# Performance work log

Measured on AMD Instinct MI355X. Metric: run time of the kernel, lower is better.

Reference implementation:

```python
import jax, jax.numpy as jnp
import numpy as np

WS = 7          # window size
DISP = 3        # WS // 2 cyclic shift displacement
HEADS = 3
HD = 32         # head dim
DIM = 96        # hidden dim (= HEADS*HD)
DS = 4          # patch-merging downscale factor
NWH = 16        # windows per spatial dim after merging (112/7)
SCALE = HD ** -0.5


def _rel_indices(ws):
    idx = np.array([[x, y] for x in range(ws) for y in range(ws)])
    return idx[None, :, :] - idx[:, None, :] + ws - 1  # (ws^2, ws^2, 2)


def _shift_mask(ws, disp, nwh, nww):
    n = ws * ws
    ul = np.zeros((n, n), np.float32)
    ul[-disp * ws:, :-disp * ws] = -np.inf
    ul[:-disp * ws, -disp * ws:] = -np.inf
    lr = np.zeros((ws, ws, ws, ws), np.float32)
    lr[:, -disp:, :, :-disp] = -np.inf
    lr[:, :-disp, :, -disp:] = -np.inf
    lr = lr.reshape(n, n)
    m = np.zeros((nwh * nww, n, n), np.float32)
    m[-nww:] += ul            # last row of windows: upper/lower mask
    m[nww - 1::nww] += lr     # last column of windows: left/right mask
    return m

REL = jnp.asarray(_rel_indices(WS))                       # (49,49,2) int
SHIFT_MASK = jnp.asarray(_shift_mask(WS, DISP, NWH, NWH))  # (256,49,49)


def _layernorm(x, g, b):
    mu = jnp.mean(x, axis=-1, keepdims=True)
    var = jnp.var(x, axis=-1, keepdims=True)
    return (x - mu) * jax.lax.rsqrt(var + 1e-5) * g + b


def _window_attention(y, wqkv, pos_tab, wo, bo, shifted):
    # y: (b, nh, nw, DIM)
    if shifted:
        y = jnp.roll(y, (-DISP, -DISP), axis=(1, 2))
    b, nh, nw, _ = y.shape
    nwh, nww = nh // WS, nw // WS
    qkv = y @ wqkv  # (b, nh, nw, 3*DIM); last dim layout [q|k|v]
    qkv = qkv.reshape(b, nwh, WS, nww, WS, 3, HEADS, HD)
    qkv = qkv.transpose(5, 0, 6, 1, 3, 2, 4, 7).reshape(3, b, HEADS, nwh * nww, WS * WS, HD)
    q, k, v = qkv[0], qkv[1], qkv[2]
    dots = jnp.einsum('bhwid,bhwjd->bhwij', q, k) * SCALE  # (b,h,nwin,49,49)
    dots = dots + pos_tab[REL[..., 0], REL[..., 1]]        # relative pos bias
    if shifted:
        dots = dots + SHIFT_MASK[None, None]
    attn = jax.nn.softmax(dots, axis=-1)
    o = jnp.einsum('bhwij,bhwjd->bhwid', attn, v)
    o = o.reshape(b, HEADS, nwh, nww, WS, WS, HD)
    o = o.transpose(0, 2, 4, 3, 5, 1, 6).reshape(b, nh, nw, HEADS * HD)
    o = o @ wo + bo
    if shifted:
        o = jnp.roll(o, (DISP, DISP), axis=(1, 2))
    return o


def setup_inputs() -> dict:
    key = jax.random.key(0)
    ks = jax.random.split(key, 8)
    B, C, H, W = 16, 3, 448, 448
    s = 0.02
    return {
        'x': jax.random.normal(ks[0], (B, C, H, W), jnp.float32),
        'pm_w': jax.random.normal(ks[1], (C * DS * DS, DIM), jnp.float32) * s,
        'pm_b': jnp.zeros((DIM,), jnp.float32),
        'ln1_g': jnp.ones((2, DIM), jnp.float32),
        'ln1_b': jnp.zeros((2, DIM), jnp.float32),
        'qkv_w': jax.random.normal(ks[2], (2, DIM, 3 * HEADS * HD), jnp.float32) * s,
        'pos': jax.random.normal(ks[3], (2, 2 * WS - 1, 2 * WS - 1), jnp.float32),
        'out_w': jax.random.normal(ks[4], (2, HEADS * HD, DIM), jnp.float32) * s,
        'out_b': jnp.zeros((2, DIM), jnp.float32),
        'ln2_g': jnp.ones((2, DIM), jnp.float32),
        'ln2_b': jnp.zeros((2, DIM), jnp.float32),
        'ff1_w': jax.random.normal(ks[5], (2, DIM, 4 * DIM), jnp.float32) * s,
        'ff1_b': jnp.zeros((2, 4 * DIM), jnp.float32),
        'ff2_w': jax.random.normal(ks[6], (2, 4 * DIM, DIM), jnp.float32) * s,
        'ff2_b': jnp.zeros((2, DIM), jnp.float32),
    }


def reference(x, pm_w, pm_b, ln1_g, ln1_b, qkv_w, pos, out_w, out_b,
              ln2_g, ln2_b, ff1_w, ff1_b, ff2_w, ff2_b):
    b, c, h, w = x.shape
    # PatchMerging: Unfold(k=s=DS) orders channels as (c, kh, kw)
    xp = x.reshape(b, c, h // DS, DS, w // DS, DS)
    xp = xp.transpose(0, 2, 4, 1, 3, 5).reshape(b, h // DS, w // DS, c * DS * DS)
    xp = xp @ pm_w + pm_b  # (b, 112, 112, DIM)
    for i, shifted in enumerate((False, True)):
        y = _layernorm(xp, ln1_g[i], ln1_b[i])
        xp = xp + _window_attention(y, qkv_w[i], pos[i], out_w[i], out_b[i], shifted)
        y = _layernorm(xp, ln2_g[i], ln2_b[i])
        y = jax.nn.gelu(y @ ff1_w[i] + ff1_b[i], approximate=False) @ ff2_w[i] + ff2_b[i]
        xp = xp + y
    return xp.transpose(0, 3, 1, 2)  # (b, DIM, 112, 112)
```

## Files before the change

### kernel.cpp

```cpp
#include <hip/hip_runtime.h>
#include <hip/hip_bf16.h>

#define HW 112
#define NPIX (HW*HW)
#define NTOK_TOTAL (16*NPIX)
#define SCALE_ATTN 0.17677669529663689f

typedef short bf16x8 __attribute__((ext_vector_type(8)));
typedef float f32x4 __attribute__((ext_vector_type(4)));

__device__ __forceinline__ short f2bf(float f) {
    __hip_bfloat16 h = __float2bfloat16(f);
    return *reinterpret_cast<short*>(&h);
}

__device__ __forceinline__ float gelu_tanh(float x) {
    float t  = x * x;
    float m1 = fmaf(0.071354816f, t, 1.5957691f);
    float e  = __expf(x * m1);
    float r  = __builtin_amdgcn_rcpf(e + 1.0f);
    return fmaf(-x, r, x);
}

__device__ __forceinline__ void gload_lds16(const short* g, short* l) {
    __builtin_amdgcn_global_load_lds(
        (__attribute__((address_space(1))) void*)g,
        (__attribute__((address_space(3))) void*)l,
        16, 0, 0);
}

__global__ __launch_bounds__(256) void patch_merge_kernel(
    const float* __restrict__ x, const float* __restrict__ pm_w,
    const float* __restrict__ pm_b, float* __restrict__ xp)
{
    __shared__ float w_lds[48*96];
    __shared__ float in_lds[16*52];
    __shared__ float b_lds[96];
    const int t = threadIdx.x;
    const int jt = blockIdx.x, i = blockIdx.y, b = blockIdx.z;
    const int j0 = jt * 16;

    for (int e = t; e < 48*96; e += 256) w_lds[e] = pm_w[e];
    if (t < 96) b_lds[t] = pm_b[t];
    for (int e = t; e < 768; e += 256) {
        int r = e >> 6, col = e & 63;
        int c = r >> 2, kh = r & 3;
        float v = x[(((size_t)(b*3 + c))*448 + (4*i + kh))*448 + 4*j0 + col];
        in_lds[(col >> 2)*52 + c*16 + kh*4 + (col & 3)] = v;
    }
    __syncthreads();
    for (int e = t; e < 16*96; e += 256) {
        int pos = e / 96, ch = e % 96;
        float acc = b_lds[ch];
        #pragma unroll
        for (int k = 0; k < 48; ++k)
            acc = fmaf(in_lds[pos*52 + k], w_lds[k*96 + ch], acc);
        xp[((size_t)((b*HW + i)*HW) + j0 + pos)*96 + ch] = acc;
    }
}

__global__ __launch_bounds__(256) void prep_weights_kernel(
    const float* __restrict__ ff1, const float* __restrict__ ff2,
    const float* __restrict__ qkv_w, const float* __restrict__ out_w,
    short* __restrict__ wF,
    short* __restrict__ qkvT, short* __restrict__ outT)
{
    int i = blockIdx.x * 256 + threadIdx.x;
    if (i < 147456) {
        int l = i / 73728, r = i % 73728;
        int c = r / 18432, r2 = r % 18432;
        int half = r2 / 9216, r3 = r2 % 9216;
        int f = r3 / 512, L = (r3 % 512) / 8, j = r3 % 8;
        int ks = f / 6, n = f % 6;
        float val;
        if (half == 0) {
            int k  = ks*32 + (L >> 4)*8 + j;
            int ng = c*96 + n*16 + (L & 15);
            val = ff1[(size_t)l*36864 + (size_t)k*384 + ng];
        } else {
            int kg = c*96 + ks*32 + (L >> 4)*8 + j;
            int ng = n*16 + (L & 15);
            val = ff2[(size_t)l*36864 + (size_t)kg*96 + ng];
        }
        wF[i] = f2bf(val);
    } else if (i < 202752) {
        int j = i - 147456;
        int l = j / 27648, r = j % 27648, n = r / 96, k = r % 96;
        float v = qkv_w[(size_t)l*27648 + k*288 + n];
        if (n < 96) v *= SCALE_ATTN;
        qkvT[j] = f2bf(v);
    } else if (i < 221184) {
        int j = i - 202752;
        int l = j / 9216, r = j % 9216, n = r / 96, k = r % 96;
        outT[j] = f2bf(out_w[(size_t)l*9216 + k*96 + n]);
    }
}

template<bool SHIFTED>
__global__ __launch_bounds__(192) void attn_mfma_kernel(
    float* __restrict__ xp,
    const float* __restrict__ ln_g, const float* __restrict__ ln_b,
    const short* __restrict__ qkvT,
    const float* __restrict__ pos_tab,
    const short* __restrict__ outT,
    const float* __restrict__ out_b)
{
    __shared__ short bufA[13824];
    __shared__ short qk_s[13824];
    __shared__ short vT_s[6912];
    __shared__ float pos_l[169];
    __shared__ float ob_s[96];
    __shared__ float lng[96], lnb[96];

    const int t = threadIdx.x;
    const int lane = t & 63;
    const int h = t >> 6;
    const int l15 = lane & 15, lhi = lane >> 4;
    const int wh = blockIdx.x >> 4, ww = blockIdx.x & 15;
    const int b = blockIdx.y;
    const int SH = SHIFTED ? 3 : 0;

    if (t < 169) pos_l[t] = pos_tab[t];
    if (t < 96) { lng[t] = ln_g[t]; lnb[t] = ln_b[t]; ob_s[t] = out_b[t]; }
    __syncthreads();

    {
        const int part = t & 3;
        for (int row = t >> 2; row < 49; row += 48) {
            int ti = (row*37) >> 8, tj = row - ti*7;
            int gi = wh*7 + ti + SH; if (gi >= HW) gi -= HW;
            int gj = ww*7 + tj + SH; if (gj >= HW) gj -= HW;
            const float* src = xp + ((size_t)((b*HW + gi)*HW + gj))*96 + part*24;
            float v[24];
            #pragma unroll
            for (int q4 = 0; q4 < 6; ++q4) {
                float4 vv = *reinterpret_cast<const float4*>(src + q4*4);
                v[q4*4+0]=vv.x; v[q4*4+1]=vv.y; v[q4*4+2]=vv.z; v[q4*4+3]=vv.w;
            }
            float s = 0.f, s2 = 0.f;
            #pragma unroll
            for (int j = 0; j < 24; ++j) { s += v[j]; s2 += v[j]*v[j]; }
            s  += __shfl_xor(s, 1);  s  += __shfl_xor(s, 2);
            s2 += __shfl_xor(s2, 1); s2 += __shfl_xor(s2, 2);
            float mu = s * (1.f/96.f);
            float var = s2 * (1.f/96.f) - mu*mu;
            float rs = rsqrtf(var + 1e-5f);
            unsigned* yw = reinterpret_cast<unsigned*>(bufA) + row*52 + part*12;
            #pragma unroll
            for (int j = 0; j < 12; ++j) {
                int c = part*24 + 2*j;
                float lo = (v[2*j]   - mu)*rs*lng[c]   + lnb[c];
                float hi = (v[2*j+1] - mu)*rs*lng[c+1] + lnb[c+1];
                yw[j] = (unsigned)(unsigned short)f2bf(lo) |
                        ((unsigned)(unsigned short)f2bf(hi) << 16);
            }
        }
        for (int e = t; e < 15*52; e += 192)
            reinterpret_cast<unsigned*>(bufA)[(49 + e/52)*52 + e%52] = 0u;
    }
    __syncthreads();

    {
        f32x4 acc[3][2][4];
        #pragma unroll
        for (int p = 0; p < 3; ++p)
            #pragma unroll
            for (int s = 0; s < 2; ++s)
                #pragma unroll
                for (int m = 0; m < 4; ++m)
                    { acc[p][s][m][0]=0.f; acc[p][s][m][1]=0.f; acc[p][s][m][2]=0.f; acc[p][s][m][3]=0.f; }
        #pragma unroll
        for (int ks = 0; ks < 3; ++ks) {
            bf16x8 a[4];
            #pragma unroll
            for (int m = 0; m < 4; ++m)
                a[m] = *reinterpret_cast<const bf16x8*>(&bufA[(m*16 + l15)*104 + ks*32 + lhi*8]);
            #pragma unroll
            for (int p = 0; p < 3; ++p)
                #pragma unroll
                for (int s = 0; s < 2; ++s) {
                    bf16x8 bf = *reinterpret_cast<const bf16x8*>(
                        qkvT + (p*96 + h*32 + s*16 + l15)*96 + ks*32 + lhi*8);
                    #pragma unroll
                    for (int m = 0; m < 4; ++m)
                        acc[p][s][m] = __builtin_amdgcn_mfma_f32_16x16x32_bf16(
                            a[m], bf, acc[p][s][m], 0, 0, 0);
                }
        }
        #pragma unroll
        for (int p = 0; p < 3; ++p)
            #pragma unroll
            for (int s = 0; s < 2; ++s)
                #pragma unroll
                for (int m = 0; m < 4; ++m)
                    #pragma unroll
                    for (int r = 0; r < 4; ++r) {
                        int tok = m*16 + lhi*4 + r;
                        int c = s*16 + l15;
                        short val = f2bf(acc[p][s][m][r]);
                        if (p == 0)      qk_s[h*4608 + tok*72 + c] = val;
                        else if (p == 1) qk_s[h*4608 + tok*72 + 32 + c] = val;
                        else             vT_s[h*2304 + c*72 + tok] = val;
                    }
    }
    __syncthreads();

    float pv[4][4][4];
    {
        f32x4 sacc[4][4];
        #pragma unroll
        for (int m = 0; m < 4; ++m)
            #pragma unroll
            for (int n = 0; n < 4; ++n)
                { sacc[m][n][0]=0.f; sacc[m][n][1]=0.f; sacc[m][n][2]=0.f; sacc[m][n][3]=0.f; }
        bf16x8 aq[4], bk[4];
        #pragma unroll
        for (int m = 0; m < 4; ++m)
            aq[m] = *reinterpret_cast<const bf16x8*>(&qk_s[h*4608 + (m*16 + l15)*72 + lhi*8]);
        #pragma unroll
        for (int n = 0; n < 4; ++n)
            bk[n] = *reinterpret_cast<const bf16x8*>(&qk_s[h*4608 + (n*16 + l15)*72 + 32 + lhi*8]);
        #pragma unroll
        for (int m = 0; m < 4; ++m)
            #pragma unroll
            for (int n = 0; n < 4; ++n)
                sacc[m][n] = __builtin_amdgcn_mfma_f32_16x16x32_bf16(aq[m], bk[n], sacc[m][n], 0, 0, 0);

        #pragma unroll
        for (int m = 0; m < 4; ++m)
            #pragma unroll
            for (int n = 0; n < 4; ++n)
                #pragma unroll
                for (int r = 0; r < 4; ++r) {
                    int i = m*16 + lhi*4 + r, j = n*16 + l15;
                    float v;
                    if (i >= 49 || j >= 49) v = -1e30f;
                    else {
                        int xi = (i*37) >> 8, yi = i - xi*7;
                        int xj = (j*37) >> 8, yj = j - xj*7;
                        v = sacc[m][n][r] + pos_l[(xj - xi + 6)*13 + (yj - yi + 6)];
                        if (SHIFTED) {
                            if (wh == 15 && ((xi >= 4) != (xj >= 4))) v = -1e30f;
                            if (ww == 15 && ((yi >= 4) != (yj >= 4))) v = -1e30f;
                        }
                    }
                    pv[m][n][r] = v;
                }
    }
    #pragma unroll
    for (int m = 0; m < 4; ++m)
        #pragma unroll
        for (int r = 0; r < 4; ++r) {
            float mx = fmaxf(fmaxf(pv[m][0][r], pv[m][1][r]), fmaxf(pv[m][2][r], pv[m][3][r]));
            mx = fmaxf(mx, __shfl_xor(mx, 1)); mx = fmaxf(mx, __shfl_xor(mx, 2));
            mx = fmaxf(mx, __shfl_xor(mx, 4)); mx = fmaxf(mx, __shfl_xor(mx, 8));
            float e0 = __expf(pv[m][0][r] - mx), e1 = __expf(pv[m][1][r] - mx);
            float e2 = __expf(pv[m][2][r] - mx), e3 = __expf(pv[m][3][r] - mx);
            float s = e0 + e1 + e2 + e3;
            s += __shfl_xor(s, 1); s += __shfl_xor(s, 2);
            s += __shfl_xor(s, 4); s += __shfl_xor(s, 8);
            float inv = 1.f / s;
            pv[m][0][r] = e0*inv; pv[m][1][r] = e1*inv;
            pv[m][2][r] = e2*inv; pv[m][3][r] = e3*inv;
        }
    #pragma unroll
    for (int m = 0; m < 4; ++m)
        #pragma unroll
        for (int n = 0; n < 4; ++n)
            #pragma unroll
            for (int r = 0; r < 4; ++r)
                bufA[h*4608 + (m*16 + lhi*4 + r)*72 + n*16 + l15] = f2bf(pv[m][n][r]);

    f32x4 oacc[2][4];
    #pragma unroll
    for (int n = 0; n < 2; ++n)
        #pragma unroll
        for (int m = 0; m < 4; ++m)
            { oacc[n][m][0]=0.f; oacc[n][m][1]=0.f; oacc[n][m][2]=0.f; oacc[n][m][3]=0.f; }
    #pragma unroll
    for (int ks = 0; ks < 2; ++ks) {
        bf16x8 ap[4], bv[2];
        #pragma unroll
        for (int m = 0; m < 4; ++m)
            ap[m] = *reinterpret_cast<const bf16x8*>(&bufA[h*4608 + (m*16 + l15)*72 + ks*32 + lhi*8]);
        #pragma unroll
        for (int n = 0; n < 2; ++n)
            bv[n] = *reinterpret_cast<const bf16x8*>(&vT_s[h*2304 + (n*16 + l15)*72 + ks*32 + lhi*8]);
        #pragma unroll
        for (int n = 0; n < 2; ++n)
            #pragma unroll
            for (int m = 0; m < 4; ++m)
                oacc[n][m] = __builtin_amdgcn_mfma_f32_16x16x32_bf16(ap[m], bv[n], oacc[n][m], 0, 0, 0);
    }
    __syncthreads();
    #pragma unroll
    for (int n = 0; n < 2; ++n)
        #pragma unroll
        for (int m = 0; m < 4; ++m)
            #pragma unroll
            for (int r = 0; r < 4; ++r)
                bufA[(m*16 + lhi*4 + r)*104 + h*32 + n*16 + l15] = f2bf(oacc[n][m][r]);
    __syncthreads();

    {
        f32x4 pacc[2][4];
        #pragma unroll
        for (int n = 0; n < 2; ++n)
            #pragma unroll
            for (int m = 0; m < 4; ++m)
                { pacc[n][m][0]=0.f; pacc[n][m][1]=0.f; pacc[n][m][2]=0.f; pacc[n][m][3]=0.f; }
        #pragma unroll
        for (int ks = 0; ks < 3; ++ks) {
            bf16x8 ao[4], bw[2];
            #pragma unroll
            for (int m = 0; m < 4; ++m)
                ao[m] = *reinterpret_cast<const bf16x8*>(&bufA[(m*16 + l15)*104 + ks*32 + lhi*8]);
            #pragma unroll
            for (int n = 0; n < 2; ++n)
                bw[n] = *reinterpret_cast<const bf16x8*>(
                    outT + ((h*2 + n)*16 + l15)*96 + ks*32 + lhi*8);
            #pragma unroll
            for (int n = 0; n < 2; ++n)
                #pragma unroll
                for (int m = 0; m < 4; ++m)
                    pacc[n][m] = __builtin_amdgcn_mfma_f32_16x16x32_bf16(ao[m], bw[n], pacc[n][m], 0, 0, 0);
        }
        #pragma unroll
        for (int m = 0; m < 4; ++m)
            #pragma unroll
            for (int r = 0; r < 4; ++r) {
                int tok = m*16 + lhi*4 + r;
                if (tok < 49) {
                    int ti = (tok*37) >> 8, tj = tok - ti*7;
                    int gi = wh*7 + ti + SH; if (gi >= HW) gi -= HW;
                    int gj = ww*7 + tj + SH; if (gj >= HW) gj -= HW;
                    float* dst = xp + ((size_t)((b*HW + gi)*HW + gj))*96;
                    #pragma unroll
                    for (int n = 0; n < 2; ++n) {
                        int ch = (h*2 + n)*16 + l15;
                        dst[ch] += pacc[n][m][r] + ob_s[ch];
                    }
                }
            }
    }
}

__global__ __launch_bounds__(256) void ff_mfma_kernel(
    float* __restrict__ xp,
    const float* __restrict__ ln_g, const float* __restrict__ ln_b,
    const short* __restrict__ wF,
    const float* __restrict__ b1,
    const float* __restrict__ b2)
{
    __shared__ short wbuf[18432];
    __shared__ short h_s[128*104];

    const int t = threadIdx.x;
    const int lane = t & 63;
    const int wv = t >> 6;
    const int l15 = lane & 15, lhi = (lane >> 4) & 3;
    const size_t tok0 = (size_t)blockIdx.x * 128 + wv*32;

    #pragma unroll
    for (int k = 0; k < 9; ++k) {
        int f = k*4 + wv;
        gload_lds16(wF + f*512 + lane*8, &wbuf[f*512]);
    }

    bf16x8 y[2][3];
    {
        float g[24], bb[24];
        #pragma unroll
        for (int ks = 0; ks < 3; ++ks)
            #pragma unroll
            for (int q = 0; q < 2; ++q) {
                float4 gv = *reinterpret_cast<const float4*>(ln_g + ks*32 + lhi*8 + q*4);
                float4 bv = *reinterpret_cast<const float4*>(ln_b + ks*32 + lhi*8 + q*4);
                g[ks*8+q*4+0]=gv.x; g[ks*8+q*4+1]=gv.y; g[ks*8+q*4+2]=gv.z; g[ks*8+q*4+3]=gv.w;
                bb[ks*8+q*4+0]=bv.x; bb[ks*8+q*4+1]=bv.y; bb[ks*8+q*4+2]=bv.z; bb[ks*8+q*4+3]=bv.w;
            }
        #pragma unroll
        for (int m = 0; m < 2; ++m) {
            const float* src = xp + (tok0 + m*16 + l15)*96 + lhi*8;
            float v[24];
            #pragma unroll
            for (int ks = 0; ks < 3; ++ks) {
                float4 a0 = *reinterpret_cast<const float4*>(src + ks*32);
                float4 a1 = *reinterpret_cast<const float4*>(src + ks*32 + 4);
                v[ks*8+0]=a0.x; v[ks*8+1]=a0.y; v[ks*8+2]=a0.z; v[ks*8+3]=a0.w;
                v[ks*8+4]=a1.x; v[ks*8+5]=a1.y; v[ks*8+6]=a1.z; v[ks*8+7]=a1.w;
            }
            float s = 0.f, s2 = 0.f;
            #pragma unroll
            for (int j = 0; j < 24; ++j) { s += v[j]; s2 += v[j]*v[j]; }
            s  += __shfl_xor(s, 16);  s  += __shfl_xor(s, 32);
            s2 += __shfl_xor(s2, 16); s2 += __shfl_xor(s2, 32);
            float mu = s * (1.f/96.f);
            float var = s2 * (1.f/96.f) - mu*mu;
            float rs = rsqrtf(var + 1e-5f);
            #pragma unroll
            for (int ks = 0; ks < 3; ++ks) {
                bf16x8 yy;
                #pragma unroll
                for (int j = 0; j < 8; ++j)
                    yy[j] = f2bf((v[ks*8+j] - mu)*rs*g[ks*8+j] + bb[ks*8+j]);
                y[m][ks] = yy;
            }
        }
    }

    f32x4 acc2[2][6];
    #pragma unroll
    for (int m = 0; m < 2; ++m)
        #pragma unroll
        for (int n = 0; n < 6; ++n)
            { acc2[m][n][0]=0.f; acc2[m][n][1]=0.f; acc2[m][n][2]=0.f; acc2[m][n][3]=0.f; }

    asm volatile("s_waitcnt vmcnt(0)" ::: "memory");
    __syncthreads();

    for (int c = 0; c < 4; ++c) {
        f32x4 acc1[2][6];
        #pragma unroll
        for (int m = 0; m < 2; ++m)
            #pragma unroll
            for (int n = 0; n < 6; ++n)
                { acc1[m][n][0]=0.f; acc1[m][n][1]=0.f; acc1[m][n][2]=0.f; acc1[m][n][3]=0.f; }
        #pragma unroll
        for (int ks = 0; ks < 3; ++ks)
            #pragma unroll
            for (int n = 0; n < 6; ++n) {
                bf16x8 bw = *reinterpret_cast<const bf16x8*>(
                    &wbuf[(ks*6 + n)*512 + lane*8]);
                #pragma unroll
                for (int m = 0; m < 2; ++m)
                    acc1[m][n] = __builtin_amdgcn_mfma_f32_16x16x32_bf16(
                        y[m][ks], bw, acc1[m][n], 0, 0, 0);
            }

        #pragma unroll
        for (int n = 0; n < 6; ++n) {
            float bias = b1[c*96 + n*16 + l15];
            #pragma unroll
            for (int m = 0; m < 2; ++m)
                #pragma unroll
                for (int r = 0; r < 4; ++r) {
                    float hv = gelu_tanh(acc1[m][n][r] + bias);
                    int row = wv*32 + m*16 + lhi*4 + r;
                    h_s[row*104 + n*16 + l15] = f2bf(hv);
                }
        }

        #pragma unroll
        for (int ks = 0; ks < 3; ++ks) {
            bf16x8 ah[2];
            #pragma unroll
            for (int m = 0; m < 2; ++m)
                ah[m] = *reinterpret_cast<const bf16x8*>(
                    &h_s[(wv*32 + m*16 + l15)*104 + ks*32 + lhi*8]);
            #pragma unroll
            for (int n = 0; n < 6; ++n) {
                bf16x8 bw = *reinterpret_cast<const bf16x8*>(
                    &wbuf[9216 + (ks*6 + n)*512 + lane*8]);
                #pragma unroll
                for (int m = 0; m < 2; ++m)
                    acc2[m][n] = __builtin_amdgcn_mfma_f32_16x16x32_bf16(
                        ah[m], bw, acc2[m][n], 0, 0, 0);
            }
        }

        if (c < 3) {
            __syncthreads();
            #pragma unroll
            for (int k = 0; k < 9; ++k) {
                int f = k*4 + wv;
                gload_lds16(wF + (c + 1)*18432 + f*512 + lane*8, &wbuf[f*512]);
            }
            asm volatile("s_waitcnt vmcnt(0)" ::: "memory");
            __syncthreads();
        }
    }

    float b2v[6];
    #pragma unroll
    for (int n = 0; n < 6; ++n) b2v[n] = b2[n*16 + l15];
    #pragma unroll
    for (int m = 0; m < 2; ++m)
        #pragma unroll
        for (int r = 0; r < 4; ++r) {
            float* dst = xp + (tok0 + m*16 + lhi*4 + r)*96 + l15;
            #pragma unroll
            for (int n = 0; n < 6; ++n)
                dst[n*16] += acc2[m][n][r] + b2v[n];
        }
}

__global__ __launch_bounds__(256) void out_kernel(
    const float* __restrict__ xp, float* __restrict__ out)
{
    __shared__ float tile[64*100];
    const int t = threadIdx.x;
    const int b = blockIdx.y;
    const int p0 = blockIdx.x * 64;
    for (int e = t; e < 64*24; e += 256) {
        int r = e / 24, p = e % 24;
        *reinterpret_cast<float4*>(&tile[r*100 + p*4]) =
            *reinterpret_cast<const float4*>(xp + ((size_t)b*NPIX + p0 + r)*96 + p*4);
    }
    __syncthreads();
    for (int e = t; e < 96*64; e += 256) {
        int ch = e >> 6, p = e & 63;
        out[((size_t)(b*96 + ch))*NPIX + p0 + p] = tile[p*100 + ch];
    }
}

extern "C" void kernel_launch(void* const* d_in, const int* in_sizes, int n_in,
                              void* d_out, int out_size, void* d_ws, size_t ws_size,
                              hipStream_t stream)
{
    (void)in_sizes; (void)n_in; (void)out_size; (void)ws_size;
    const float* x     = (const float*)d_in[0];
    const float* pm_w  = (const float*)d_in[1];
    const float* pm_b  = (const float*)d_in[2];
    const float* ln1_g = (const float*)d_in[3];
    const float* ln1_b = (const float*)d_in[4];
    const float* qkv_w = (const float*)d_in[5];
    const float* pos   = (const float*)d_in[6];
    const float* out_w = (const float*)d_in[7];
    const float* out_b = (const float*)d_in[8];
    const float* ln2_g = (const float*)d_in[9];
    const float* ln2_b = (const float*)d_in[10];
    const float* ff1_w = (const float*)d_in[11];
    const float* ff1_b = (const float*)d_in[12];
    const float* ff2_w = (const float*)d_in[13];
    const float* ff2_b = (const float*)d_in[14];

    float* xp    = (float*)d_ws;
    short* wF_b  = (short*)(xp + (size_t)NTOK_TOTAL * 96);
    short* qkvT_b = wF_b + 147456;
    short* outT_b = qkvT_b + 2*288*96;

    prep_weights_kernel<<<864, 256, 0, stream>>>(ff1_w, ff2_w, qkv_w, out_w,
                                                 wF_b, qkvT_b, outT_b);
    patch_merge_kernel<<<dim3(7, 112, 16), 256, 0, stream>>>(x, pm_w, pm_b, xp);

    for (int L = 0; L < 2; ++L) {
        if (L == 0)
            attn_mfma_kernel<false><<<dim3(256, 16), 192, 0, stream>>>(
                xp, ln1_g, ln1_b, qkvT_b, pos, outT_b, out_b);
        else
            attn_mfma_kernel<true><<<dim3(256, 16), 192, 0, stream>>>(
                xp, ln1_g + 96, ln1_b + 96, qkvT_b + 27648, pos + 169,
                outT_b + 9216, out_b + 96);
        ff_mfma_kernel<<<1568, 256, 0, stream>>>(
            xp, ln2_g + L*96, ln2_b + L*96,
            wF_b + (size_t)L*73728, ff1_b + L*384, ff2_b + L*96);
    }
    out_kernel<<<dim3(196, 16), 256, 0, stream>>>(xp, (float*)d_out);
}
```

Baseline: 523.5 us.

## Double-buffer FF weight chunks and widen patch-merge blocks to full rows

New measurement: 537.3 us. +2.7%, slower.

```diff
diff --git a/kernel.cpp b/kernel.cpp
--- a/kernel.cpp
+++ b/kernel.cpp
@@ -34,28 +34,27 @@
     const float* __restrict__ pm_b, float* __restrict__ xp)
 {
     __shared__ float w_lds[48*96];
-    __shared__ float in_lds[16*52];
+    __shared__ float in_lds[112*52];
     __shared__ float b_lds[96];
     const int t = threadIdx.x;
-    const int jt = blockIdx.x, i = blockIdx.y, b = blockIdx.z;
-    const int j0 = jt * 16;
+    const int i = blockIdx.x, b = blockIdx.y;
 
     for (int e = t; e < 48*96; e += 256) w_lds[e] = pm_w[e];
     if (t < 96) b_lds[t] = pm_b[t];
-    for (int e = t; e < 768; e += 256) {
-        int r = e >> 6, col = e & 63;
+    for (int e = t; e < 12*448; e += 256) {
+        int r = e / 448, col = e % 448;
         int c = r >> 2, kh = r & 3;
-        float v = x[(((size_t)(b*3 + c))*448 + (4*i + kh))*448 + 4*j0 + col];
+        float v = x[(((size_t)(b*3 + c))*448 + (4*i + kh))*448 + col];
         in_lds[(col >> 2)*52 + c*16 + kh*4 + (col & 3)] = v;
     }
     __syncthreads();
-    for (int e = t; e < 16*96; e += 256) {
+    for (int e = t; e < 112*96; e += 256) {
         int pos = e / 96, ch = e % 96;
         float acc = b_lds[ch];
         #pragma unroll
         for (int k = 0; k < 48; ++k)
             acc = fmaf(in_lds[pos*52 + k], w_lds[k*96 + ch], acc);
-        xp[((size_t)((b*HW + i)*HW) + j0 + pos)*96 + ch] = acc;
+        xp[((size_t)((b*HW + i)*HW) + pos)*96 + ch] = acc;
     }
 }
 
@@ -352,7 +351,8 @@
     const float* __restrict__ b1,
     const float* __restrict__ b2)
 {
-    __shared__ short wbuf[18432];
+    __shared__ short wbuf1[9216];
+    __shared__ short wbuf2[2][9216];
     __shared__ short h_s[128*104];
 
     const int t = threadIdx.x;
@@ -361,10 +361,18 @@
     const int l15 = lane & 15, lhi = (lane >> 4) & 3;
     const size_t tok0 = (size_t)blockIdx.x * 128 + wv*32;
 
-    #pragma unroll
-    for (int k = 0; k < 9; ++k) {
-        int f = k*4 + wv;
-        gload_lds16(wF + f*512 + lane*8, &wbuf[f*512]);
+    if (wv < 2) {
+        #pragma unroll
+        for (int k = 0; k < 9; ++k) {
+            int f = k*2 + wv;
+            gload_lds16(wF + f*512 + lane*8, &wbuf1[f*512]);
+        }
+    } else {
+        #pragma unroll
+        for (int k = 0; k < 9; ++k) {
+            int f = k*2 + (wv - 2);
+            gload_lds16(wF + 9216 + f*512 + lane*8, &wbuf2[0][f*512]);
+        }
     }
 
     bf16x8 y[2][3];
@@ -420,6 +428,16 @@
     __syncthreads();
 
     for (int c = 0; c < 4; ++c) {
+        const int p = c & 1;
+        if (c < 3 && wv >= 2) {
+            #pragma unroll
+            for (int k = 0; k < 9; ++k) {
+                int f = k*2 + (wv - 2);
+                gload_lds16(wF + (c + 1)*18432 + 9216 + f*512 + lane*8,
+                            &wbuf2[p ^ 1][f*512]);
+            }
+        }
+
         f32x4 acc1[2][6];
         #pragma unroll
         for (int m = 0; m < 2; ++m)
@@ -431,12 +449,21 @@
             #pragma unroll
             for (int n = 0; n < 6; ++n) {
                 bf16x8 bw = *reinterpret_cast<const bf16x8*>(
-                    &wbuf[(ks*6 + n)*512 + lane*8]);
+                    &wbuf1[(ks*6 + n)*512 + lane*8]);
                 #pragma unroll
                 for (int m = 0; m < 2; ++m)
                     acc1[m][n] = __builtin_amdgcn_mfma_f32_16x16x32_bf16(
                         y[m][ks], bw, acc1[m][n], 0, 0, 0);
             }
+
+        __syncthreads();
+        if (c < 3 && wv < 2) {
+            #pragma unroll
+            for (int k = 0; k < 9; ++k) {
+                int f = k*2 + wv;
+                gload_lds16(wF + (c + 1)*18432 + f*512 + lane*8, &wbuf1[f*512]);
+            }
+        }
 
         #pragma unroll
         for (int n = 0; n < 6; ++n) {
@@ -461,7 +488,7 @@
             #pragma unroll
             for (int n = 0; n < 6; ++n) {
                 bf16x8 bw = *reinterpret_cast<const bf16x8*>(
-                    &wbuf[9216 + (ks*6 + n)*512 + lane*8]);
+                    &wbuf2[p][(ks*6 + n)*512 + lane*8]);
                 #pragma unroll
                 for (int m = 0; m < 2; ++m)
                     acc2[m][n] = __builtin_amdgcn_mfma_f32_16x16x32_bf16(
@@ -470,12 +497,6 @@
         }
 
         if (c < 3) {
-            __syncthreads();
-            #pragma unroll
-            for (int k = 0; k < 9; ++k) {
-                int f = k*4 + wv;
-                gload_lds16(wF + (c + 1)*18432 + f*512 + lane*8, &wbuf[f*512]);
-            }
             asm volatile("s_waitcnt vmcnt(0)" ::: "memory");
             __syncthreads();
         }
@@ -542,7 +563,7 @@
 
     prep_weights_kernel<<<864, 256, 0, stream>>>(ff1_w, ff2_w, qkv_w, out_w,
                                                  wF_b, qkvT_b, outT_b);
-    patch_merge_kernel<<<dim3(7, 112, 16), 256, 0, stream>>>(x, pm_w, pm_b, xp);
+    patch_merge_kernel<<<dim3(112, 16), 256, 0, stream>>>(x, pm_w, pm_b, xp);
 
     for (int L = 0; L < 2; ++L) {
         if (L == 0)
```
